# Performance work log

Measured on AMD Instinct MI355X. Metric: run time of the kernel, lower is better.

Reference implementation:

```python
import jax, jax.numpy as jnp
import numpy as np

N_NODES = 50000
N_EDGES = 640000
N_FEAT = 512
HIDDEN = 128
N_CLASSES = 64


def setup_inputs() -> dict:
    key = jax.random.key(0)
    k1, k2, k3, k4, k5, k6 = jax.random.split(key, 6)
    x = jax.random.normal(k1, (N_NODES, N_FEAT), dtype=jnp.float32)
    edge_index = jax.random.randint(k2, (2, N_EDGES), 0, N_NODES, dtype=jnp.int32)
    # GCNConv weights (glorot-ish scale) and biases
    W1 = jax.random.normal(k3, (N_FEAT, HIDDEN), dtype=jnp.float32) / np.sqrt(N_FEAT)
    b1 = jnp.zeros((HIDDEN,), dtype=jnp.float32)
    W2 = jax.random.normal(k4, (HIDDEN, N_CLASSES), dtype=jnp.float32) / np.sqrt(HIDDEN)
    b2 = jnp.zeros((N_CLASSES,), dtype=jnp.float32)
    return {"x": x, "edge_index": edge_index, "W1": W1, "b1": b1, "W2": W2, "b2": b2}


def reference(x, edge_index, W1, b1, W2, b2):
    N = x.shape[0]
    # Add self-loops (PyG GCNConv default)
    loop = jnp.arange(N, dtype=edge_index.dtype)
    src = jnp.concatenate([edge_index[0], loop])
    dst = jnp.concatenate([edge_index[1], loop])
    # Symmetric normalization: deg computed over targets incl. self-loops
    deg = jax.ops.segment_sum(jnp.ones(src.shape[0], dtype=x.dtype), dst, num_segments=N)
    dinv = jax.lax.rsqrt(deg)  # deg >= 1 thanks to self-loops
    norm = dinv[src] * dinv[dst]  # [E+N]

    def gcn_conv(h, W, b):
        h = h @ W                          # dense transform first (smaller msg dim)
        msg = h[src] * norm[:, None]       # gather + normalize
        return jax.ops.segment_sum(msg, dst, num_segments=N) + b  # scatter-add + bias

    h = jax.nn.relu(gcn_conv(x, W1, b1))
    # F.dropout with training=False is identity (eval mode)
    return gcn_conv(h, W2, b2)
```

## Files before the change

kernel.cpp:

```cpp
#include <hip/hip_runtime.h>


#define NNODES 50000
#define NEDGES 640000
#define NFEAT 512
#define NHID 128
#define NCLS 64

typedef _Float16 f16x8 __attribute__((ext_vector_type(8)));
typedef _Float16 f16x2 __attribute__((ext_vector_type(2)));
typedef float f32x4 __attribute__((ext_vector_type(4)));

__global__ void k_zero2(int* __restrict__ a, int* __restrict__ b, int n) {
  int i = blockIdx.x * blockDim.x + threadIdx.x;
  if (i < n) { a[i] = 0; b[i] = 0; }
}

__global__ void k_hist(const int* __restrict__ dst, int* __restrict__ indeg, int E) {
  int i = blockIdx.x * blockDim.x + threadIdx.x;
  if (i < E) atomicAdd(&indeg[dst[i]], 1);
}

__global__ void k_dinv(const int* __restrict__ indeg, float* __restrict__ dinv, int n) {
  int i = blockIdx.x * blockDim.x + threadIdx.x;
  if (i < n) dinv[i] = 1.0f / sqrtf((float)(indeg[i] + 1));
}

__global__ void k_scan_block(const int* __restrict__ indeg, int* __restrict__ row_start,
                             int* __restrict__ blocksum, int n) {
  __shared__ int sdata[256];
  int t = threadIdx.x;
  int base = blockIdx.x * 1024 + t * 4;
  int v[4];
#pragma unroll
  for (int j = 0; j < 4; ++j) {
    int idx = base + j;
    int d = (idx < n) ? indeg[idx] : 0;
    v[j] = (d + 3) & ~3;
  }
  int tsum = v[0] + v[1] + v[2] + v[3];
  sdata[t] = tsum;
  __syncthreads();
  for (int off = 1; off < 256; off <<= 1) {
    int x = (t >= off) ? sdata[t - off] : 0;
    __syncthreads();
    sdata[t] += x;
    __syncthreads();
  }
  int excl = sdata[t] - tsum;
  if (t == 255) blocksum[blockIdx.x] = sdata[255];
  int run = excl;
#pragma unroll
  for (int j = 0; j < 4; ++j) {
    if (base + j <= n) { row_start[base + j] = run; run += v[j]; }
  }
}

__global__ void k_scan_top(const int* __restrict__ blocksum, int* __restrict__ blockoff, int nb) {
  if (threadIdx.x == 0 && blockIdx.x == 0) {
    int run = 0;
    for (int i = 0; i < nb; ++i) { blockoff[i] = run; run += blocksum[i]; }
  }
}

__global__ void k_scan_add(int* __restrict__ row_start, const int* __restrict__ blockoff, int n) {
  int i = blockIdx.x * blockDim.x + threadIdx.x;
  if (i <= n) row_start[i] += blockoff[i >> 10];
}

__global__ void k_pad(const int* __restrict__ indeg, const int* __restrict__ row_start,
                      int* __restrict__ csr_src, float* __restrict__ csr_norm, int n) {
  int i = blockIdx.x * blockDim.x + threadIdx.x;
  if (i < n) {
    int d = indeg[i];
    int p = (d + 3) & ~3;
    int b = row_start[i];
    for (int j = d; j < p; ++j) { csr_src[b + j] = i; csr_norm[b + j] = 0.f; }
  }
}

__global__ void k_scatter(const int* __restrict__ src, const int* __restrict__ dst,
                          const int* __restrict__ row_start, int* __restrict__ cursor,
                          const float* __restrict__ dinv, int* __restrict__ csr_src,
                          float* __restrict__ csr_norm, int E) {
  int e = blockIdx.x * blockDim.x + threadIdx.x;
  if (e < E) {
    int s = src[e], d = dst[e];
    int pos = atomicAdd(&cursor[d], 1);
    int idx = row_start[d] + pos;
    csr_src[idx] = s;
    csr_norm[idx] = dinv[s] * dinv[d];
  }
}

__global__ void k_wcvt(const float* __restrict__ W, _Float16* __restrict__ Wt_hi,
                       _Float16* __restrict__ Wt_lo, int K, int Nc) {
  int i = blockIdx.x * blockDim.x + threadIdx.x;
  if (i < K * Nc) {
    int k = i / Nc, n = i % Nc;
    float v = W[i];
    _Float16 h = (_Float16)v;
    Wt_hi[(size_t)n * K + k] = h;
    Wt_lo[(size_t)n * K + k] = (_Float16)((v - (float)h) * 1024.0f);
  }
}

__global__ __launch_bounds__(256) void k_gemm1(const float* __restrict__ A,
                                               const _Float16* __restrict__ Bhi,
                                               const _Float16* __restrict__ Blo,
                                               float* __restrict__ C, int M) {
  constexpr int K = NFEAT, N = NHID;
  const int wid = threadIdx.x >> 6, lane = threadIdx.x & 63;
  const int wy = wid >> 1, wx = wid & 1;
  const int r0 = blockIdx.x * 64 + wy * 32;
  const int c0 = wx * 64;
  const int lrow = lane & 15, koff = (lane >> 4) * 8;

  f32x4 acc_h[2][4] = {};
  f32x4 acc_l[2][4] = {};
  f16x8 bh[2][4], bl[2][4], ah[2][2], al[2][2];

  auto loadB = [&](int buf, int k0) {
#pragma unroll
    for (int cf = 0; cf < 4; ++cf) {
      size_t off = (size_t)(c0 + cf * 16 + lrow) * K + k0 + koff;
      bh[buf][cf] = *(const f16x8*)(Bhi + off);
      bl[buf][cf] = *(const f16x8*)(Blo + off);
    }
  };
  auto loadA = [&](int buf, int k0) {
#pragma unroll
    for (int rf = 0; rf < 2; ++rf) {
      int row = r0 + rf * 16 + lrow;
      row = row < M ? row : M - 1;
      const float* p = A + (size_t)row * K + k0 + koff;
      float4 v0 = *(const float4*)p;
      float4 v1 = *(const float4*)(p + 4);
      float vv[8] = {v0.x, v0.y, v0.z, v0.w, v1.x, v1.y, v1.z, v1.w};
#pragma unroll
      for (int j = 0; j < 8; ++j) {
        _Float16 h = (_Float16)vv[j];
        ah[buf][rf][j] = h;
        al[buf][rf][j] = (_Float16)((vv[j] - (float)h) * 1024.0f);
      }
    }
  };

  loadB(0, 0);
  loadA(0, 0);
#pragma unroll
  for (int ks = 0; ks < K / 32; ++ks) {
    const int cur = ks & 1, nxt = cur ^ 1;
    if (ks + 1 < K / 32) { loadB(nxt, (ks + 1) * 32); loadA(nxt, (ks + 1) * 32); }
#pragma unroll
    for (int rf = 0; rf < 2; ++rf)
#pragma unroll
      for (int cf = 0; cf < 4; ++cf) {
        acc_h[rf][cf] = __builtin_amdgcn_mfma_f32_16x16x32_f16(ah[cur][rf], bh[cur][cf],
                                                               acc_h[rf][cf], 0, 0, 0);
        acc_l[rf][cf] = __builtin_amdgcn_mfma_f32_16x16x32_f16(ah[cur][rf], bl[cur][cf],
                                                               acc_l[rf][cf], 0, 0, 0);
        acc_l[rf][cf] = __builtin_amdgcn_mfma_f32_16x16x32_f16(al[cur][rf], bh[cur][cf],
                                                               acc_l[rf][cf], 0, 0, 0);
      }
  }

#pragma unroll
  for (int rf = 0; rf < 2; ++rf) {
    if (r0 + rf * 16 >= M) continue;
    int rbase = r0 + rf * 16 + (lane >> 4) * 4;
#pragma unroll
    for (int cf = 0; cf < 4; ++cf) {
      int col = c0 + cf * 16 + lrow;
#pragma unroll
      for (int q = 0; q < 4; ++q)
        C[(size_t)(rbase + q) * N + col] =
            acc_h[rf][cf][q] + acc_l[rf][cf][q] * (1.0f / 1024.0f);
    }
  }
}

__global__ __launch_bounds__(256) void k_gemm2(const _Float16* __restrict__ Ahi,
                                               const _Float16* __restrict__ Alo,
                                               const _Float16* __restrict__ Bhi,
                                               const _Float16* __restrict__ Blo,
                                               float* __restrict__ C, int M) {
  constexpr int K = NHID, N = NCLS;
  const int wid = threadIdx.x >> 6, lane = threadIdx.x & 63;
  const int r0 = blockIdx.x * 64 + wid * 16;
  const int lrow = lane & 15, koff = (lane >> 4) * 8;

  f32x4 acc_h[4] = {};
  f32x4 acc_l[4] = {};
  f16x8 bh[2][4], bl[2][4], ah[2], al[2];

  auto loadB = [&](int buf, int k0) {
#pragma unroll
    for (int cf = 0; cf < 4; ++cf) {
      size_t off = (size_t)(cf * 16 + lrow) * K + k0 + koff;
      bh[buf][cf] = *(const f16x8*)(Bhi + off);
      bl[buf][cf] = *(const f16x8*)(Blo + off);
    }
  };
  auto loadA = [&](int buf, int k0) {
    int row = r0 + lrow;
    row = row < M ? row : M - 1;
    size_t off = (size_t)row * K + k0 + koff;
    ah[buf] = *(const f16x8*)(Ahi + off);
    al[buf] = *(const f16x8*)(Alo + off);
  };

  loadB(0, 0);
  loadA(0, 0);
#pragma unroll
  for (int ks = 0; ks < K / 32; ++ks) {
    const int cur = ks & 1, nxt = cur ^ 1;
    if (ks + 1 < K / 32) { loadB(nxt, (ks + 1) * 32); loadA(nxt, (ks + 1) * 32); }
#pragma unroll
    for (int cf = 0; cf < 4; ++cf) {
      acc_h[cf] = __builtin_amdgcn_mfma_f32_16x16x32_f16(ah[cur], bh[cur][cf],
                                                         acc_h[cf], 0, 0, 0);
      acc_l[cf] = __builtin_amdgcn_mfma_f32_16x16x32_f16(ah[cur], bl[cur][cf],
                                                         acc_l[cf], 0, 0, 0);
      acc_l[cf] = __builtin_amdgcn_mfma_f32_16x16x32_f16(al[cur], bh[cur][cf],
                                                         acc_l[cf], 0, 0, 0);
    }
  }

  if (r0 < M) {
    int rbase = r0 + (lane >> 4) * 4;
#pragma unroll
    for (int cf = 0; cf < 4; ++cf) {
      int col = cf * 16 + lrow;
#pragma unroll
      for (int q = 0; q < 4; ++q)
        C[(size_t)(rbase + q) * N + col] = acc_h[cf][q] + acc_l[cf][q] * (1.0f / 1024.0f);
    }
  }
}

template <bool RELU, bool EMIT16>
__global__ __launch_bounds__(256) void k_agg128(
    const float* __restrict__ h, const float* __restrict__ bias,
    const int* __restrict__ row_start, const int* __restrict__ csr_src,
    const float* __restrict__ csr_norm, const float* __restrict__ dinv,
    float* __restrict__ out, _Float16* __restrict__ out_hi,
    _Float16* __restrict__ out_lo, int N) {
  int node = blockIdx.x * 4 + (threadIdx.x >> 6);
  if (node >= N) return;
  int lane = threadIdx.x & 63;
  const float2* hp = (const float2*)h;

  float dn = dinv[node];
  float2 bs = ((const float2*)bias)[lane];
  float2 sf = hp[(size_t)node * 64 + lane];
  float2 a0 = {dn * dn * sf.x + bs.x, dn * dn * sf.y + bs.y};
  float2 a1 = {0.f, 0.f}, a2 = {0.f, 0.f}, a3 = {0.f, 0.f};
  float2 a4 = {0.f, 0.f}, a5 = {0.f, 0.f}, a6 = {0.f, 0.f}, a7 = {0.f, 0.f};

  int e = row_start[node], e1 = row_start[node + 1];
#define GATH(ACC, EI)                                        \
  {                                                          \
    int s_ = csr_src[EI];                                    \
    float w_ = csr_norm[EI];                                 \
    float2 v_ = hp[(size_t)s_ * 64 + lane];                  \
    ACC.x += w_ * v_.x;                                      \
    ACC.y += w_ * v_.y;                                      \
  }
  for (; e + 8 <= e1; e += 8) {
    GATH(a0, e + 0) GATH(a1, e + 1) GATH(a2, e + 2) GATH(a3, e + 3)
    GATH(a4, e + 4) GATH(a5, e + 5) GATH(a6, e + 6) GATH(a7, e + 7)
  }
  if (e < e1) {
    GATH(a0, e + 0) GATH(a1, e + 1) GATH(a2, e + 2) GATH(a3, e + 3)
  }
#undef GATH
  float ax = ((a0.x + a1.x) + (a2.x + a3.x)) + ((a4.x + a5.x) + (a6.x + a7.x));
  float ay = ((a0.y + a1.y) + (a2.y + a3.y)) + ((a4.y + a5.y) + (a6.y + a7.y));
  if (RELU) { ax = fmaxf(ax, 0.f); ay = fmaxf(ay, 0.f); }
  if (EMIT16) {
    _Float16 hx = (_Float16)ax, hy = (_Float16)ay;
    f16x2 vh = {hx, hy};
    f16x2 vl = {(_Float16)((ax - (float)hx) * 1024.0f),
                (_Float16)((ay - (float)hy) * 1024.0f)};
    *(f16x2*)(out_hi + (size_t)node * 128 + lane * 2) = vh;
    *(f16x2*)(out_lo + (size_t)node * 128 + lane * 2) = vl;
  } else {
    ((float2*)out)[(size_t)node * 64 + lane] = {ax, ay};
  }
}

__global__ __launch_bounds__(256) void k_agg64(
    const float* __restrict__ h, const float* __restrict__ bias,
    const int* __restrict__ row_start, const int* __restrict__ csr_src,
    const float* __restrict__ csr_norm, const float* __restrict__ dinv,
    float* __restrict__ out, int N) {
  int node = blockIdx.x * 4 + (threadIdx.x >> 6);
  if (node >= N) return;
  int f = threadIdx.x & 63;
  float dn = dinv[node];
  float a0 = dn * dn * h[(size_t)node * 64 + f] + bias[f];
  float a1 = 0.f, a2 = 0.f, a3 = 0.f, a4 = 0.f, a5 = 0.f, a6 = 0.f, a7 = 0.f;
  int e = row_start[node], e1 = row_start[node + 1];
#define GATH(ACC, EI) ACC += csr_norm[EI] * h[(size_t)csr_src[EI] * 64 + f];
  for (; e + 8 <= e1; e += 8) {
    GATH(a0, e + 0) GATH(a1, e + 1) GATH(a2, e + 2) GATH(a3, e + 3)
    GATH(a4, e + 4) GATH(a5, e + 5) GATH(a6, e + 6) GATH(a7, e + 7)
  }
  if (e < e1) {
    GATH(a0, e + 0) GATH(a1, e + 1) GATH(a2, e + 2) GATH(a3, e + 3)
  }
#undef GATH
  out[(size_t)node * 64 + f] =
      ((a0 + a1) + (a2 + a3)) + ((a4 + a5) + (a6 + a7));
}

static inline size_t align256(size_t x) { return (x + 255) & ~(size_t)255; }

extern "C" void kernel_launch(void* const* d_in, const int* in_sizes, int n_in,
                              void* d_out, int out_size, void* d_ws, size_t ws_size,
                              hipStream_t stream) {
  const float* x = (const float*)d_in[0];
  const int* edge = (const int*)d_in[1];
  const float* W1 = (const float*)d_in[2];
  const float* b1 = (const float*)d_in[3];
  const float* W2 = (const float*)d_in[4];
  const float* b2 = (const float*)d_in[5];
  float* out = (float*)d_out;

  const int N = NNODES;
  const int E = NEDGES;
  const int EPAD = E + 3 * N + 256;
  const int* src = edge;
  const int* dst = edge + E;

  char* w = (char*)d_ws;
  int* indeg = (int*)w;            w += align256((size_t)N * 4);
  int* cursor = (int*)w;           w += align256((size_t)N * 4);
  float* dinv = (float*)w;         w += align256((size_t)N * 4);
  int* row_start = (int*)w;        w += align256((size_t)(N + 1) * 4);
  int* blocksum = (int*)w;         w += align256(64 * 4);
  int* blockoff = (int*)w;         w += align256(64 * 4);
  int* csr_src = (int*)w;          w += align256((size_t)EPAD * 4);
  float* csr_norm = (float*)w;     w += align256((size_t)EPAD * 4);
  _Float16* W1t_hi = (_Float16*)w; w += align256((size_t)NFEAT * NHID * 2);
  _Float16* W1t_lo = (_Float16*)w; w += align256((size_t)NFEAT * NHID * 2);
  _Float16* W2t_hi = (_Float16*)w; w += align256((size_t)NHID * NCLS * 2);
  _Float16* W2t_lo = (_Float16*)w; w += align256((size_t)NHID * NCLS * 2);
  float* h0 = (float*)w;           w += align256((size_t)N * NHID * 4);
  _Float16* h1_hi = (_Float16*)w;  w += align256((size_t)N * NHID * 2);
  _Float16* h1_lo = (_Float16*)w;  w += align256((size_t)N * NHID * 2);
  float* h2 = (float*)w;           w += align256((size_t)N * NCLS * 4);

  const int nblk_n = (N + 255) / 256;
  const int nblk_n1 = (N + 1 + 255) / 256;
  const int nblk_e = (E + 255) / 256;
  const int nblk_scan = (N + 1 + 1023) / 1024;

  k_zero2<<<nblk_n, 256, 0, stream>>>(indeg, cursor, N);
  k_hist<<<nblk_e, 256, 0, stream>>>(dst, indeg, E);
  k_dinv<<<nblk_n, 256, 0, stream>>>(indeg, dinv, N);
  k_scan_block<<<nblk_scan, 256, 0, stream>>>(indeg, row_start, blocksum, N);
  k_scan_top<<<1, 64, 0, stream>>>(blocksum, blockoff, nblk_scan);
  k_scan_add<<<nblk_n1, 256, 0, stream>>>(row_start, blockoff, N);
  k_pad<<<nblk_n, 256, 0, stream>>>(indeg, row_start, csr_src, csr_norm, N);
  k_scatter<<<nblk_e, 256, 0, stream>>>(src, dst, row_start, cursor, dinv,
                                        csr_src, csr_norm, E);

  k_wcvt<<<(NFEAT * NHID + 255) / 256, 256, 0, stream>>>(W1, W1t_hi, W1t_lo,
                                                         NFEAT, NHID);
  k_wcvt<<<(NHID * NCLS + 255) / 256, 256, 0, stream>>>(W2, W2t_hi, W2t_lo,
                                                        NHID, NCLS);

  k_gemm1<<<(N + 63) / 64, 256, 0, stream>>>(x, W1t_hi, W1t_lo, h0, N);
  k_agg128<true, true><<<(N + 3) / 4, 256, 0, stream>>>(
      h0, b1, row_start, csr_src, csr_norm, dinv, nullptr, h1_hi, h1_lo, N);
  k_gemm2<<<(N + 63) / 64, 256, 0, stream>>>(h1_hi, h1_lo, W2t_hi, W2t_lo, h2, N);
  k_agg64<<<(N + 3) / 4, 256, 0, stream>>>(h2, b2, row_start, csr_src, csr_norm,
                                           dinv, out, N);
}
```

Before: 416.1 us.

## Stage GEMM tiles through LDS with async global-to-LDS loads and fuse preprocessing kernels

Both GEMM kernels now stage A and B tiles into double-buffered, XOR-swizzled shared memory using global_load_lds, replacing the previous per-lane direct global loads. The goal is to share B-operand loads across waves and overlap the next tile's fetch with the current tile's MFMA work. The change also folds dinv computation into the scan block kernel and padding into scan_add, which removes two kernel launches. The trade-offs are more LDS per block, which may lower occupancy, and a barrier on every k-step.

```diff
diff --git a/kernel.cpp b/kernel.cpp
--- a/kernel.cpp
+++ b/kernel.cpp
@@ -11,6 +11,12 @@
 typedef _Float16 f16x2 __attribute__((ext_vector_type(2)));
 typedef float f32x4 __attribute__((ext_vector_type(4)));
 
+__device__ __forceinline__ void g2l16(const void* g, void* s) {
+  __builtin_amdgcn_global_load_lds(
+      (const __attribute__((address_space(1))) void*)g,
+      (__attribute__((address_space(3))) void*)s, 16, 0, 0);
+}
+
 __global__ void k_zero2(int* __restrict__ a, int* __restrict__ b, int n) {
   int i = blockIdx.x * blockDim.x + threadIdx.x;
   if (i < n) { a[i] = 0; b[i] = 0; }
@@ -21,13 +27,9 @@
   if (i < E) atomicAdd(&indeg[dst[i]], 1);
 }
 
-__global__ void k_dinv(const int* __restrict__ indeg, float* __restrict__ dinv, int n) {
-  int i = blockIdx.x * blockDim.x + threadIdx.x;
-  if (i < n) dinv[i] = 1.0f / sqrtf((float)(indeg[i] + 1));
-}
-
-__global__ void k_scan_block(const int* __restrict__ indeg, int* __restrict__ row_start,
-                             int* __restrict__ blocksum, int n) {
+__global__ void k_scan_block(const int* __restrict__ indeg, float* __restrict__ dinv,
+                             int* __restrict__ row_start, int* __restrict__ blocksum,
+                             int n) {
   __shared__ int sdata[256];
   int t = threadIdx.x;
   int base = blockIdx.x * 1024 + t * 4;
@@ -36,6 +38,7 @@
   for (int j = 0; j < 4; ++j) {
     int idx = base + j;
     int d = (idx < n) ? indeg[idx] : 0;
+    if (idx < n) dinv[idx] = 1.0f / sqrtf((float)(d + 1));
     v[j] = (d + 3) & ~3;
   }
   int tsum = v[0] + v[1] + v[2] + v[3];
@@ -63,19 +66,18 @@
   }
 }
 
-__global__ void k_scan_add(int* __restrict__ row_start, const int* __restrict__ blockoff, int n) {
+__global__ void k_scan_add(int* __restrict__ row_start, const int* __restrict__ blockoff,
+                           const int* __restrict__ indeg, int* __restrict__ csr_src,
+                           float* __restrict__ csr_norm, int n) {
   int i = blockIdx.x * blockDim.x + threadIdx.x;
-  if (i <= n) row_start[i] += blockoff[i >> 10];
-}
-
-__global__ void k_pad(const int* __restrict__ indeg, const int* __restrict__ row_start,
-                      int* __restrict__ csr_src, float* __restrict__ csr_norm, int n) {
-  int i = blockIdx.x * blockDim.x + threadIdx.x;
-  if (i < n) {
-    int d = indeg[i];
-    int p = (d + 3) & ~3;
-    int b = row_start[i];
-    for (int j = d; j < p; ++j) { csr_src[b + j] = i; csr_norm[b + j] = 0.f; }
+  if (i <= n) {
+    int rs = row_start[i] + blockoff[i >> 10];
+    row_start[i] = rs;
+    if (i < n) {
+      int d = indeg[i];
+      int p = (d + 3) & ~3;
+      for (int j = d; j < p; ++j) { csr_src[rs + j] = i; csr_norm[rs + j] = 0.f; }
+    }
   }
 }
 
@@ -109,72 +111,100 @@
                                                const _Float16* __restrict__ Bhi,
                                                const _Float16* __restrict__ Blo,
                                                float* __restrict__ C, int M) {
-  constexpr int K = NFEAT, N = NHID;
-  const int wid = threadIdx.x >> 6, lane = threadIdx.x & 63;
+  __shared__ char smem[49152];
+  constexpr int A_OFF = 0;
+  constexpr int BH_OFF = 16384;
+  constexpr int BL_OFF = 32768;
+  const int tid = threadIdx.x;
+  const int wid = tid >> 6, lane = tid & 63;
   const int wy = wid >> 1, wx = wid & 1;
-  const int r0 = blockIdx.x * 64 + wy * 32;
-  const int c0 = wx * 64;
-  const int lrow = lane & 15, koff = (lane >> 4) * 8;
+  const int row0 = blockIdx.x * 64;
+  const int lrow = lane & 15;
+  const int lkg = lane >> 4;
+
+  auto stage = [&](int buf, int k0) {
+#pragma unroll
+    for (int c = 0; c < 2; ++c) {
+      int idx = c * 256 + tid;
+      int row = idx >> 3;
+      int kq = (idx & 7) ^ (row & 7);
+      int gr = row0 + row; gr = gr < M ? gr : M - 1;
+      g2l16((const char*)A + (size_t)gr * 2048 + (size_t)k0 * 4 + kq * 16,
+            smem + A_OFF + buf * 8192 + ((idx & ~63) << 4));
+    }
+#pragma unroll
+    for (int c = 0; c < 2; ++c) {
+      int idx = c * 256 + tid;
+      int n = idx >> 2;
+      int kq = (idx & 3) ^ (n & 3);
+      size_t so = (size_t)n * 1024 + (size_t)k0 * 2 + kq * 16;
+      g2l16((const char*)Bhi + so, smem + BH_OFF + buf * 8192 + ((idx & ~63) << 4));
+      g2l16((const char*)Blo + so, smem + BL_OFF + buf * 8192 + ((idx & ~63) << 4));
+    }
+  };
 
   f32x4 acc_h[2][4] = {};
   f32x4 acc_l[2][4] = {};
-  f16x8 bh[2][4], bl[2][4], ah[2][2], al[2][2];
-
-  auto loadB = [&](int buf, int k0) {
-#pragma unroll
-    for (int cf = 0; cf < 4; ++cf) {
-      size_t off = (size_t)(c0 + cf * 16 + lrow) * K + k0 + koff;
-      bh[buf][cf] = *(const f16x8*)(Bhi + off);
-      bl[buf][cf] = *(const f16x8*)(Blo + off);
-    }
-  };
-  auto loadA = [&](int buf, int k0) {
+
+  stage(0, 0);
+  __syncthreads();
+  int cur = 0;
+  constexpr int NK = NFEAT / 32;
+  for (int ks = 0; ks < NK; ++ks) {
+    if (ks + 1 < NK) stage(cur ^ 1, (ks + 1) * 32);
+
+    const char* ab = smem + A_OFF + cur * 8192;
+    const char* bhb = smem + BH_OFF + cur * 8192;
+    const char* blb = smem + BL_OFF + cur * 8192;
+    f16x8 ah[2], al[2], bh[4], bl[4];
 #pragma unroll
     for (int rf = 0; rf < 2; ++rf) {
-      int row = r0 + rf * 16 + lrow;
-      row = row < M ? row : M - 1;
-      const float* p = A + (size_t)row * K + k0 + koff;
-      float4 v0 = *(const float4*)p;
-      float4 v1 = *(const float4*)(p + 4);
+      int r = wy * 32 + rf * 16 + lrow;
+      int lin = r * 128 + lkg * 32;
+      int sw = (r & 7) << 4;
+      float4 v0 = *(const float4*)(ab + (lin ^ sw));
+      float4 v1 = *(const float4*)(ab + ((lin + 16) ^ sw));
       float vv[8] = {v0.x, v0.y, v0.z, v0.w, v1.x, v1.y, v1.z, v1.w};
 #pragma unroll
       for (int j = 0; j < 8; ++j) {
         _Float16 h = (_Float16)vv[j];
-        ah[buf][rf][j] = h;
-        al[buf][rf][j] = (_Float16)((vv[j] - (float)h) * 1024.0f);
+        ah[rf][j] = h;
+        al[rf][j] = (_Float16)((vv[j] - (float)h) * 1024.0f);
       }
     }
-  };
-
-  loadB(0, 0);
-  loadA(0, 0);
-#pragma unroll
-  for (int ks = 0; ks < K / 32; ++ks) {
-    const int cur = ks & 1, nxt = cur ^ 1;
-    if (ks + 1 < K / 32) { loadB(nxt, (ks + 1) * 32); loadA(nxt, (ks + 1) * 32); }
+#pragma unroll
+    for (int cf = 0; cf < 4; ++cf) {
+      int n = wx * 64 + cf * 16 + lrow;
+      int lin = n * 64 + lkg * 16;
+      int sw = (n & 3) << 4;
+      bh[cf] = *(const f16x8*)(bhb + (lin ^ sw));
+      bl[cf] = *(const f16x8*)(blb + (lin ^ sw));
+    }
 #pragma unroll
     for (int rf = 0; rf < 2; ++rf)
 #pragma unroll
       for (int cf = 0; cf < 4; ++cf) {
-        acc_h[rf][cf] = __builtin_amdgcn_mfma_f32_16x16x32_f16(ah[cur][rf], bh[cur][cf],
+        acc_h[rf][cf] = __builtin_amdgcn_mfma_f32_16x16x32_f16(ah[rf], bh[cf],
                                                                acc_h[rf][cf], 0, 0, 0);
-        acc_l[rf][cf] = __builtin_amdgcn_mfma_f32_16x16x32_f16(ah[cur][rf], bl[cur][cf],
+        acc_l[rf][cf] = __builtin_amdgcn_mfma_f32_16x16x32_f16(ah[rf], bl[cf],
                                                                acc_l[rf][cf], 0, 0, 0);
-        acc_l[rf][cf] = __builtin_amdgcn_mfma_f32_16x16x32_f16(al[cur][rf], bh[cur][cf],
+        acc_l[rf][cf] = __builtin_amdgcn_mfma_f32_16x16x32_f16(al[rf], bh[cf],
                                                                acc_l[rf][cf], 0, 0, 0);
       }
+    if (ks + 1 < NK) { __syncthreads(); cur ^= 1; }
   }
 
 #pragma unroll
   for (int rf = 0; rf < 2; ++rf) {
-    if (r0 + rf * 16 >= M) continue;
-    int rbase = r0 + rf * 16 + (lane >> 4) * 4;
+    int rfrag = row0 + wy * 32 + rf * 16;
+    if (rfrag >= M) continue;
+    int rbase = rfrag + lkg * 4;
 #pragma unroll
     for (int cf = 0; cf < 4; ++cf) {
-      int col = c0 + cf * 16 + lrow;
+      int col = wx * 64 + cf * 16 + lrow;
 #pragma unroll
       for (int q = 0; q < 4; ++q)
-        C[(size_t)(rbase + q) * N + col] =
+        C[(size_t)(rbase + q) * NHID + col] =
             acc_h[rf][cf][q] + acc_l[rf][cf][q] * (1.0f / 1024.0f);
     }
   }
@@ -185,56 +215,78 @@
                                                const _Float16* __restrict__ Bhi,
                                                const _Float16* __restrict__ Blo,
                                                float* __restrict__ C, int M) {
-  constexpr int K = NHID, N = NCLS;
-  const int wid = threadIdx.x >> 6, lane = threadIdx.x & 63;
-  const int r0 = blockIdx.x * 64 + wid * 16;
-  const int lrow = lane & 15, koff = (lane >> 4) * 8;
+  __shared__ char smem[32768];
+  constexpr int AH_OFF = 0;
+  constexpr int AL_OFF = 8192;
+  constexpr int BH_OFF = 16384;
+  constexpr int BL_OFF = 24576;
+  const int tid = threadIdx.x;
+  const int wid = tid >> 6, lane = tid & 63;
+  const int row0 = blockIdx.x * 64;
+  const int lrow = lane & 15;
+  const int lkg = lane >> 4;
+
+  auto stage = [&](int buf, int k0) {
+    int idx = tid;
+    int row = idx >> 2;
+    int kq = (idx & 3) ^ (row & 3);
+    int gr = row0 + row; gr = gr < M ? gr : M - 1;
+    size_t aso = (size_t)gr * 256 + (size_t)k0 * 2 + kq * 16;
+    size_t bso = (size_t)row * 256 + (size_t)k0 * 2 + kq * 16;
+    int ldso = (idx & ~63) << 4;
+    g2l16((const char*)Ahi + aso, smem + AH_OFF + buf * 4096 + ldso);
+    g2l16((const char*)Alo + aso, smem + AL_OFF + buf * 4096 + ldso);
+    g2l16((const char*)Bhi + bso, smem + BH_OFF + buf * 4096 + ldso);
+    g2l16((const char*)Blo + bso, smem + BL_OFF + buf * 4096 + ldso);
+  };
 
   f32x4 acc_h[4] = {};
   f32x4 acc_l[4] = {};
-  f16x8 bh[2][4], bl[2][4], ah[2], al[2];
-
-  auto loadB = [&](int buf, int k0) {
+
+  stage(0, 0);
+  __syncthreads();
+  int cur = 0;
+  constexpr int NK = NHID / 32;
+  for (int ks = 0; ks < NK; ++ks) {
+    if (ks + 1 < NK) stage(cur ^ 1, (ks + 1) * 32);
+
+    const char* ahb = smem + AH_OFF + cur * 4096;
+    const char* alb = smem + AL_OFF + cur * 4096;
+    const char* bhb = smem + BH_OFF + cur * 4096;
+    const char* blb = smem + BL_OFF + cur * 4096;
+    int r = wid * 16 + lrow;
+    int alin = r * 64 + lkg * 16;
+    int asw = (r & 3) << 4;
+    f16x8 ah = *(const f16x8*)(ahb + (alin ^ asw));
+    f16x8 al = *(const f16x8*)(alb + (alin ^ asw));
+    f16x8 bh[4], bl[4];
 #pragma unroll
     for (int cf = 0; cf < 4; ++cf) {
-      size_t off = (size_t)(cf * 16 + lrow) * K + k0 + koff;
-      bh[buf][cf] = *(const f16x8*)(Bhi + off);
-      bl[buf][cf] = *(const f16x8*)(Blo + off);
-    }
-  };
-  auto loadA = [&](int buf, int k0) {
-    int row = r0 + lrow;
-    row = row < M ? row : M - 1;
-    size_t off = (size_t)row * K + k0 + koff;
-    ah[buf] = *(const f16x8*)(Ahi + off);
-    al[buf] = *(const f16x8*)(Alo + off);
-  };
-
-  loadB(0, 0);
-  loadA(0, 0);
-#pragma unroll
-  for (int ks = 0; ks < K / 32; ++ks) {
-    const int cur = ks & 1, nxt = cur ^ 1;
-    if (ks + 1 < K / 32) { loadB(nxt, (ks + 1) * 32); loadA(nxt, (ks + 1) * 32); }
+      int n = cf * 16 + lrow;
+      int lin = n * 64 + lkg * 16;
+      int sw = (n & 3) << 4;
+      bh[cf] = *(const f16x8*)(bhb + (lin ^ sw));
+      bl[cf] = *(const f16x8*)(blb + (lin ^ sw));
+    }
 #pragma unroll
     for (int cf = 0; cf < 4; ++cf) {
-      acc_h[cf] = __builtin_amdgcn_mfma_f32_16x16x32_f16(ah[cur], bh[cur][cf],
-                                                         acc_h[cf], 0, 0, 0);
-      acc_l[cf] = __builtin_amdgcn_mfma_f32_16x16x32_f16(ah[cur], bl[cur][cf],
-                                                         acc_l[cf], 0, 0, 0);
-      acc_l[cf] = __builtin_amdgcn_mfma_f32_16x16x32_f16(al[cur], bh[cur][cf],
-                                                         acc_l[cf], 0, 0, 0);
-    }
-  }
-
-  if (r0 < M) {
-    int rbase = r0 + (lane >> 4) * 4;
+      acc_h[cf] = __builtin_amdgcn_mfma_f32_16x16x32_f16(ah, bh[cf], acc_h[cf], 0, 0, 0);
+      acc_l[cf] = __builtin_amdgcn_mfma_f32_16x16x32_f16(ah, bl[cf], acc_l[cf], 0, 0, 0);
+      acc_l[cf] = __builtin_amdgcn_mfma_f32_16x16x32_f16(al, bh[cf], acc_l[cf], 0, 0, 0);
+    }
+    if (ks + 1 < NK) { __syncthreads(); cur ^= 1; }
+  }
+
+  int rfrag = row0 + wid * 16;
+  if (rfrag < M) {
+    int rbase = rfrag + lkg * 4;
 #pragma unroll
     for (int cf = 0; cf < 4; ++cf) {
       int col = cf * 16 + lrow;
 #pragma unroll
       for (int q = 0; q < 4; ++q)
-        C[(size_t)(rbase + q) * N + col] = acc_h[cf][q] + acc_l[cf][q] * (1.0f / 1024.0f);
+        C[(size_t)(rbase + q) * NCLS + col] =
+            acc_h[cf][q] + acc_l[cf][q] * (1.0f / 1024.0f);
     }
   }
 }
@@ -359,11 +411,10 @@
 
   k_zero2<<<nblk_n, 256, 0, stream>>>(indeg, cursor, N);
   k_hist<<<nblk_e, 256, 0, stream>>>(dst, indeg, E);
-  k_dinv<<<nblk_n, 256, 0, stream>>>(indeg, dinv, N);
-  k_scan_block<<<nblk_scan, 256, 0, stream>>>(indeg, row_start, blocksum, N);
+  k_scan_block<<<nblk_scan, 256, 0, stream>>>(indeg, dinv, row_start, blocksum, N);
   k_scan_top<<<1, 64, 0, stream>>>(blocksum, blockoff, nblk_scan);
-  k_scan_add<<<nblk_n1, 256, 0, stream>>>(row_start, blockoff, N);
-  k_pad<<<nblk_n, 256, 0, stream>>>(indeg, row_start, csr_src, csr_norm, N);
+  k_scan_add<<<nblk_n1, 256, 0, stream>>>(row_start, blockoff, indeg, csr_src,
+                                          csr_norm, N);
   k_scatter<<<nblk_e, 256, 0, stream>>>(src, dst, row_start, cursor, dinv,
                                         csr_src, csr_norm, E);
 
```

Measured after the change: 350.8 us. -15.7%, faster.
